# Kernel tuning notes

Hardware: AMD Instinct MI355X
Metric: run time of the kernel (lower is better)

The kernel has to match this reference:

```python
import jax, jax.numpy as jnp
import numpy as np

N, K, D = 8192, 4096, 256


def setup_inputs() -> dict:
    key = jax.random.key(0)
    kx, kc, kw = jax.random.split(key, 3)
    x = jax.random.normal(kx, (N, D), dtype=jnp.float32)
    centers = jax.random.normal(kc, (K, D), dtype=jnp.float32)
    w = jax.random.normal(kw, (K,), dtype=jnp.float32)
    # bandwidth chosen so exp(-sigma * d2) stays in a healthy range for
    # Gaussian data where E[||x-c||^2] ~= 2*D
    sigma = jnp.asarray(1.0 / (2.0 * D), dtype=jnp.float32)
    return {"x": x, "centers": centers, "w": w, "sigma": sigma}


def reference(x, centers, w, sigma):
    # phi[n,k] = exp(-sigma * ||x_n - c_k||^2), computed via the GEMM
    x2 = jnp.sum(x * x, axis=-1, keepdims=True)          # [N,1]
    c2 = jnp.sum(centers * centers, axis=-1)             # [K]
    d2 = x2 + c2 - 2.0 * jnp.einsum('nd,kd->nk', x, centers)  # [N,K]
    d2 = jnp.maximum(d2, 0.0)  # clamp tiny negative round-off
    phi = jnp.exp(-sigma * d2)                           # [N,K]
    # (w * phi).sum(1) == phi @ w
    return jnp.einsum('nk,k->n', phi, w)                 # [N]
```

## Files before the change

### kernel.cpp

```cpp
#include <hip/hip_runtime.h>

#define NROWS 8192
#define NCENT 4096
#define DIM   256

#define AS1 __attribute__((address_space(1)))
#define AS3 __attribute__((address_space(3)))

typedef short bf16x8 __attribute__((ext_vector_type(8)));
typedef float f32x4  __attribute__((ext_vector_type(4)));

__device__ inline unsigned short f2bf(float f) {
    unsigned u = __float_as_uint(f);
    return (unsigned short)((u + 0x7fffu + ((u >> 16) & 1u)) >> 16);
}

__global__ __launch_bounds__(256) void prep_kernel(const float* __restrict__ x,
                                                   const float* __restrict__ c,
                                                   float* __restrict__ norms,
                                                   unsigned short* __restrict__ xbf,
                                                   unsigned short* __restrict__ cbf,
                                                   float* __restrict__ out) {
    const int t = threadIdx.x, lane = t & 63;
    if (blockIdx.x < NROWS / 256) out[blockIdx.x * 256 + t] = 0.0f;
    const int wbase = (blockIdx.x * 4 + (t >> 6)) * 4;
    #pragma unroll
    for (int rr = 0; rr < 4; ++rr) {
        const int gw = wbase + rr;
        const float* src;
        unsigned short* dst;
        if (gw < NROWS) { src = x + (size_t)gw * DIM;           dst = xbf + (size_t)gw * DIM; }
        else            { src = c + (size_t)(gw - NROWS) * DIM; dst = cbf + (size_t)(gw - NROWS) * DIM; }
        float4 v = ((const float4*)src)[lane];
        ushort4 b;
        b.x = f2bf(v.x); b.y = f2bf(v.y); b.z = f2bf(v.z); b.w = f2bf(v.w);
        ((ushort4*)dst)[lane] = b;
        float s = v.x * v.x + v.y * v.y + v.z * v.z + v.w * v.w;
        #pragma unroll
        for (int m = 32; m; m >>= 1) s += __shfl_xor(s, m);
        if (lane == 0) norms[gw] = s;
    }
}

#define BUFH (128 * 32)

__global__ __launch_bounds__(256, 3) void rbf_mfma(const unsigned short* __restrict__ xbf,
                                                   const unsigned short* __restrict__ cbf,
                                                   const float* __restrict__ w,
                                                   const float* __restrict__ sigp,
                                                   const float* __restrict__ norms,
                                                   float* __restrict__ out) {
    __shared__ __align__(16) short As[2 * BUFH];
    __shared__ __align__(16) short Bs[2 * BUFH];

    const int t    = threadIdx.x;
    const int wave = t >> 6, lane = t & 63;
    const int m0   = blockIdx.y * 128;
    const int n0   = blockIdx.x * 128;
    const int wy   = wave >> 1, wx = wave & 1;
    const int lr   = lane & 15;
    const int g    = lane >> 4;

    const int r_in = lane >> 2;
    const int c_l  = (lane & 3) ^ ((r_in >> 1) & 3);
    const unsigned short* ga0 = xbf + (size_t)(m0 + 32 * wave + r_in) * DIM + c_l * 8;
    const unsigned short* ga1 = ga0 + 16 * DIM;
    const unsigned short* gb0 = cbf + (size_t)(n0 + 32 * wave + r_in) * DIM + c_l * 8;
    const unsigned short* gb1 = gb0 + 16 * DIM;
    short* la0 = As + (32 * wave) * 32;
    short* lb0 = Bs + (32 * wave) * 32;

#define STAGE(buf, kk) do {                                                                  \
        const int ko_ = (kk) * 32;                                                           \
        __builtin_amdgcn_global_load_lds((const AS1 void*)(ga0 + ko_),                       \
                                         (AS3 void*)(la0 + (buf) * BUFH), 16, 0, 0);         \
        __builtin_amdgcn_global_load_lds((const AS1 void*)(ga1 + ko_),                       \
                                         (AS3 void*)(la0 + (buf) * BUFH + 16 * 32), 16, 0, 0);\
        __builtin_amdgcn_global_load_lds((const AS1 void*)(gb0 + ko_),                       \
                                         (AS3 void*)(lb0 + (buf) * BUFH), 16, 0, 0);         \
        __builtin_amdgcn_global_load_lds((const AS1 void*)(gb1 + ko_),                       \
                                         (AS3 void*)(lb0 + (buf) * BUFH + 16 * 32), 16, 0, 0);\
    } while (0)

    int aoff[4], boff[4];
    #pragma unroll
    for (int i = 0; i < 4; ++i) {
        int r = 64 * wy + 16 * i + lr;
        aoff[i] = r * 32 + ((g ^ ((r >> 1) & 3)) * 8);
    }
    #pragma unroll
    for (int j = 0; j < 4; ++j) {
        int r = 64 * wx + 16 * j + lr;
        boff[j] = r * 32 + ((g ^ ((r >> 1) & 3)) * 8);
    }

    f32x4 acc[4][4];
    #pragma unroll
    for (int i = 0; i < 4; ++i)
        #pragma unroll
        for (int j = 0; j < 4; ++j) acc[i][j] = f32x4{0, 0, 0, 0};

    STAGE(0, 0);
    __syncthreads();

    #pragma unroll
    for (int kk = 0; kk < DIM / 32; ++kk) {
        const int cur = kk & 1;
        if (kk < DIM / 32 - 1) STAGE(cur ^ 1, kk + 1);

        const short* Ab = As + cur * BUFH;
        const short* Bb = Bs + cur * BUFH;
        bf16x8 a[4], b[4];
        #pragma unroll
        for (int i = 0; i < 4; ++i) a[i] = *(const bf16x8*)(Ab + aoff[i]);
        #pragma unroll
        for (int j = 0; j < 4; ++j) b[j] = *(const bf16x8*)(Bb + boff[j]);
        #pragma unroll
        for (int i = 0; i < 4; ++i)
            #pragma unroll
            for (int j = 0; j < 4; ++j)
                acc[i][j] = __builtin_amdgcn_mfma_f32_16x16x32_bf16(a[i], b[j], acc[i][j], 0, 0, 0);

        __syncthreads();
    }
#undef STAGE

    const float s2 = sigp[0] * 1.4426950408889634f;
    const float* x2 = norms;
    const float* c2 = norms + NROWS;

    float c2v[4], wv[4];
    #pragma unroll
    for (int j = 0; j < 4; ++j) {
        int n = n0 + 64 * wx + 16 * j + lr;
        c2v[j] = c2[n];
        wv[j]  = w[n];
    }
    float4 x2v[4];
    #pragma unroll
    for (int i = 0; i < 4; ++i)
        x2v[i] = *(const float4*)(x2 + m0 + 64 * wy + 16 * i + 4 * g);

    #pragma unroll
    for (int i = 0; i < 4; ++i) {
        const int mbase = m0 + 64 * wy + 16 * i + 4 * g;
        float rs[4] = {0.f, 0.f, 0.f, 0.f};
        #pragma unroll
        for (int j = 0; j < 4; ++j) {
            #pragma unroll
            for (int r = 0; r < 4; ++r) {
                float x2r = (r == 0) ? x2v[i].x : (r == 1) ? x2v[i].y : (r == 2) ? x2v[i].z : x2v[i].w;
                float d2 = x2r + c2v[j] - 2.0f * acc[i][j][r];
                float e  = fminf(-s2 * d2, 0.0f);
                rs[r] += wv[j] * exp2f(e);
            }
        }
        #pragma unroll
        for (int r = 0; r < 4; ++r) {
            rs[r] += __shfl_xor(rs[r], 1);
            rs[r] += __shfl_xor(rs[r], 2);
            rs[r] += __shfl_xor(rs[r], 4);
            rs[r] += __shfl_xor(rs[r], 8);
        }
        if (lr == 0) {
            #pragma unroll
            for (int r = 0; r < 4; ++r) atomicAdd(&out[mbase + r], rs[r]);
        }
    }
}

__global__ __launch_bounds__(256) void norms_kernel(const float* __restrict__ x,
                                                    const float* __restrict__ c,
                                                    float* __restrict__ ws) {
    int t = threadIdx.x, lane = t & 63;
    int gw = blockIdx.x * 4 + (t >> 6);
    const float* src;
    float* dst;
    if (gw < NROWS) { src = x + (size_t)gw * DIM;           dst = ws + gw; }
    else            { src = c + (size_t)(gw - NROWS) * DIM; dst = ws + gw; }
    float4 v = ((const float4*)src)[lane];
    float s = v.x * v.x + v.y * v.y + v.z * v.z + v.w * v.w;
    #pragma unroll
    for (int m = 32; m; m >>= 1) s += __shfl_xor(s, m);
    if (lane == 0) *dst = s;
}

__global__ __launch_bounds__(256) void rbf_kernel(const float* __restrict__ x,
                                                  const float* __restrict__ cent,
                                                  const float* __restrict__ w,
                                                  const float* __restrict__ sigp,
                                                  const float* __restrict__ norms,
                                                  float* __restrict__ out) {
    __shared__ __align__(16) short xs[64 * 32];
    __shared__ __align__(16) short cs[64 * 32];
    const int t = threadIdx.x;
    const int m0 = blockIdx.y * 64, n0 = blockIdx.x * 64;
    const int srow = t >> 2, seg = t & 3;
    const int pchunk = seg ^ ((srow >> 1) & 3);
    const int sidx = srow * 32 + pchunk * 8;
    const float* xg = x    + (size_t)(m0 + srow) * DIM + seg * 8;
    const float* cg = cent + (size_t)(n0 + srow) * DIM + seg * 8;
    const int lane = t & 63, wave = t >> 6;
    const int lr = lane & 15, lg = lane >> 4;
    const int arow = 16 * wave + lr;
    const int aidx = arow * 32 + ((lg ^ ((arow >> 1) & 3)) * 8);
    f32x4 acc[4] = {f32x4{0,0,0,0}, f32x4{0,0,0,0}, f32x4{0,0,0,0}, f32x4{0,0,0,0}};
    for (int k0 = 0; k0 < DIM; k0 += 32) {
        float4 f0 = *(const float4*)(xg + k0);
        float4 f1 = *(const float4*)(xg + k0 + 4);
        float4 g0 = *(const float4*)(cg + k0);
        float4 g1 = *(const float4*)(cg + k0 + 4);
        __syncthreads();
        union { unsigned short s[8]; int4 v; } ux, uc;
        ux.s[0]=f2bf(f0.x); ux.s[1]=f2bf(f0.y); ux.s[2]=f2bf(f0.z); ux.s[3]=f2bf(f0.w);
        ux.s[4]=f2bf(f1.x); ux.s[5]=f2bf(f1.y); ux.s[6]=f2bf(f1.z); ux.s[7]=f2bf(f1.w);
        uc.s[0]=f2bf(g0.x); uc.s[1]=f2bf(g0.y); uc.s[2]=f2bf(g0.z); uc.s[3]=f2bf(g0.w);
        uc.s[4]=f2bf(g1.x); uc.s[5]=f2bf(g1.y); uc.s[6]=f2bf(g1.z); uc.s[7]=f2bf(g1.w);
        *(int4*)(xs + sidx) = ux.v;
        *(int4*)(cs + sidx) = uc.v;
        __syncthreads();
        bf16x8 a = *(const bf16x8*)(xs + aidx);
        #pragma unroll
        for (int bt = 0; bt < 4; ++bt) {
            const int brow = 16 * bt + lr;
            bf16x8 b = *(const bf16x8*)(cs + brow * 32 + ((lg ^ ((brow >> 1) & 3)) * 8));
            acc[bt] = __builtin_amdgcn_mfma_f32_16x16x32_bf16(a, b, acc[bt], 0, 0, 0);
        }
    }
    const float sigma = sigp[0];
    const float* x2 = norms;
    const float* c2 = norms + NROWS;
    const int rbase = m0 + 16 * wave + lg * 4;
    float x2v[4];
    #pragma unroll
    for (int r = 0; r < 4; ++r) x2v[r] = x2[rbase + r];
    float rs[4] = {0.f, 0.f, 0.f, 0.f};
    #pragma unroll
    for (int bt = 0; bt < 4; ++bt) {
        const int col = n0 + 16 * bt + lr;
        const float c2v = c2[col];
        const float wvv = w[col];
        #pragma unroll
        for (int r = 0; r < 4; ++r) {
            float d2 = x2v[r] + c2v - 2.0f * acc[bt][r];
            d2 = fmaxf(d2, 0.0f);
            rs[r] += wvv * __expf(-sigma * d2);
        }
    }
    #pragma unroll
    for (int r = 0; r < 4; ++r) {
        rs[r] += __shfl_xor(rs[r], 1);
        rs[r] += __shfl_xor(rs[r], 2);
        rs[r] += __shfl_xor(rs[r], 4);
        rs[r] += __shfl_xor(rs[r], 8);
    }
    if (lr == 0) {
        #pragma unroll
        for (int r = 0; r < 4; ++r) atomicAdd(&out[rbase + r], rs[r]);
    }
}

extern "C" void kernel_launch(void* const* d_in, const int* in_sizes, int n_in,
                              void* d_out, int out_size, void* d_ws, size_t ws_size,
                              hipStream_t stream) {
    const float* x    = (const float*)d_in[0];
    const float* cent = (const float*)d_in[1];
    const float* w    = (const float*)d_in[2];
    const float* sig  = (const float*)d_in[3];
    float* out = (float*)d_out;

    const size_t norms_elems = NROWS + NCENT;
    const size_t xbf_off  = norms_elems * sizeof(float);
    const size_t cbf_off  = xbf_off + (size_t)NROWS * DIM * sizeof(unsigned short);
    const size_t ws_need  = cbf_off + (size_t)NCENT * DIM * sizeof(unsigned short);

    if (ws_size >= ws_need) {
        float* norms = (float*)d_ws;
        unsigned short* xbf = (unsigned short*)((char*)d_ws + xbf_off);
        unsigned short* cbf = (unsigned short*)((char*)d_ws + cbf_off);
        prep_kernel<<<(NROWS + NCENT) / 16, 256, 0, stream>>>(x, cent, norms, xbf, cbf, out);
        rbf_mfma<<<dim3(NCENT / 128, NROWS / 128), 256, 0, stream>>>(xbf, cbf, w, sig, norms, out);
    } else {
        float* norms = (float*)d_ws;
        hipMemsetAsync(d_out, 0, (size_t)out_size * sizeof(float), stream);
        norms_kernel<<<(NROWS + NCENT) / 4, 256, 0, stream>>>(x, cent, norms);
        rbf_kernel<<<dim3(NCENT / 64, NROWS / 64), 256, 0, stream>>>(x, cent, w, sig, norms, out);
    }
}
```

Before: 108.8 us.

## Load MFMA operands directly from global memory into registers, dropping LDS staging

Removes the shared-memory double buffer and the global_load_lds staging. Each wave now loads its bf16 A/B fragments straight from global memory into registers, with a two-deep register ping-pong across K steps. This eliminates LDS traffic and the per-step barriers, but each wave re-fetches data that other waves in the block used to share. Global loads become 16-byte per-lane row-strided accesses that lean on L1/L2 for reuse.

```diff
diff --git a/kernel.cpp b/kernel.cpp
--- a/kernel.cpp
+++ b/kernel.cpp
@@ -3,9 +3,6 @@
 #define NROWS 8192
 #define NCENT 4096
 #define DIM   256
-
-#define AS1 __attribute__((address_space(1)))
-#define AS3 __attribute__((address_space(3)))
 
 typedef short bf16x8 __attribute__((ext_vector_type(8)));
 typedef float f32x4  __attribute__((ext_vector_type(4)));
@@ -42,17 +39,12 @@
     }
 }
 
-#define BUFH (128 * 32)
-
 __global__ __launch_bounds__(256, 3) void rbf_mfma(const unsigned short* __restrict__ xbf,
                                                    const unsigned short* __restrict__ cbf,
                                                    const float* __restrict__ w,
                                                    const float* __restrict__ sigp,
                                                    const float* __restrict__ norms,
                                                    float* __restrict__ out) {
-    __shared__ __align__(16) short As[2 * BUFH];
-    __shared__ __align__(16) short Bs[2 * BUFH];
-
     const int t    = threadIdx.x;
     const int wave = t >> 6, lane = t & 63;
     const int m0   = blockIdx.y * 128;
@@ -61,38 +53,14 @@
     const int lr   = lane & 15;
     const int g    = lane >> 4;
 
-    const int r_in = lane >> 2;
-    const int c_l  = (lane & 3) ^ ((r_in >> 1) & 3);
-    const unsigned short* ga0 = xbf + (size_t)(m0 + 32 * wave + r_in) * DIM + c_l * 8;
-    const unsigned short* ga1 = ga0 + 16 * DIM;
-    const unsigned short* gb0 = cbf + (size_t)(n0 + 32 * wave + r_in) * DIM + c_l * 8;
-    const unsigned short* gb1 = gb0 + 16 * DIM;
-    short* la0 = As + (32 * wave) * 32;
-    short* lb0 = Bs + (32 * wave) * 32;
-
-#define STAGE(buf, kk) do {                                                                  \
-        const int ko_ = (kk) * 32;                                                           \
-        __builtin_amdgcn_global_load_lds((const AS1 void*)(ga0 + ko_),                       \
-                                         (AS3 void*)(la0 + (buf) * BUFH), 16, 0, 0);         \
-        __builtin_amdgcn_global_load_lds((const AS1 void*)(ga1 + ko_),                       \
-                                         (AS3 void*)(la0 + (buf) * BUFH + 16 * 32), 16, 0, 0);\
-        __builtin_amdgcn_global_load_lds((const AS1 void*)(gb0 + ko_),                       \
-                                         (AS3 void*)(lb0 + (buf) * BUFH), 16, 0, 0);         \
-        __builtin_amdgcn_global_load_lds((const AS1 void*)(gb1 + ko_),                       \
-                                         (AS3 void*)(lb0 + (buf) * BUFH + 16 * 32), 16, 0, 0);\
-    } while (0)
-
-    int aoff[4], boff[4];
-    #pragma unroll
-    for (int i = 0; i < 4; ++i) {
-        int r = 64 * wy + 16 * i + lr;
-        aoff[i] = r * 32 + ((g ^ ((r >> 1) & 3)) * 8);
-    }
-    #pragma unroll
-    for (int j = 0; j < 4; ++j) {
-        int r = 64 * wx + 16 * j + lr;
-        boff[j] = r * 32 + ((g ^ ((r >> 1) & 3)) * 8);
-    }
+    const unsigned short* ga[4];
+    const unsigned short* gb[4];
+    #pragma unroll
+    for (int i = 0; i < 4; ++i)
+        ga[i] = xbf + (size_t)(m0 + 64 * wy + 16 * i + lr) * DIM + g * 8;
+    #pragma unroll
+    for (int j = 0; j < 4; ++j)
+        gb[j] = cbf + (size_t)(n0 + 64 * wx + 16 * j + lr) * DIM + g * 8;
 
     f32x4 acc[4][4];
     #pragma unroll
@@ -100,30 +68,39 @@
         #pragma unroll
         for (int j = 0; j < 4; ++j) acc[i][j] = f32x4{0, 0, 0, 0};
 
-    STAGE(0, 0);
-    __syncthreads();
-
-    #pragma unroll
-    for (int kk = 0; kk < DIM / 32; ++kk) {
-        const int cur = kk & 1;
-        if (kk < DIM / 32 - 1) STAGE(cur ^ 1, kk + 1);
-
-        const short* Ab = As + cur * BUFH;
-        const short* Bb = Bs + cur * BUFH;
-        bf16x8 a[4], b[4];
-        #pragma unroll
-        for (int i = 0; i < 4; ++i) a[i] = *(const bf16x8*)(Ab + aoff[i]);
-        #pragma unroll
-        for (int j = 0; j < 4; ++j) b[j] = *(const bf16x8*)(Bb + boff[j]);
+    bf16x8 a0[4], b0[4], a1[4], b1[4];
+
+    #pragma unroll
+    for (int i = 0; i < 4; ++i) a0[i] = *(const bf16x8*)(ga[i]);
+    #pragma unroll
+    for (int j = 0; j < 4; ++j) b0[j] = *(const bf16x8*)(gb[j]);
+
+    #pragma unroll
+    for (int kk = 0; kk < 8; kk += 2) {
+        if (kk + 1 < 8) {
+            #pragma unroll
+            for (int i = 0; i < 4; ++i) a1[i] = *(const bf16x8*)(ga[i] + (kk + 1) * 32);
+            #pragma unroll
+            for (int j = 0; j < 4; ++j) b1[j] = *(const bf16x8*)(gb[j] + (kk + 1) * 32);
+        }
         #pragma unroll
         for (int i = 0; i < 4; ++i)
             #pragma unroll
             for (int j = 0; j < 4; ++j)
-                acc[i][j] = __builtin_amdgcn_mfma_f32_16x16x32_bf16(a[i], b[j], acc[i][j], 0, 0, 0);
-
-        __syncthreads();
-    }
-#undef STAGE
+                acc[i][j] = __builtin_amdgcn_mfma_f32_16x16x32_bf16(a0[i], b0[j], acc[i][j], 0, 0, 0);
+
+        if (kk + 2 < 8) {
+            #pragma unroll
+            for (int i = 0; i < 4; ++i) a0[i] = *(const bf16x8*)(ga[i] + (kk + 2) * 32);
+            #pragma unroll
+            for (int j = 0; j < 4; ++j) b0[j] = *(const bf16x8*)(gb[j] + (kk + 2) * 32);
+        }
+        #pragma unroll
+        for (int i = 0; i < 4; ++i)
+            #pragma unroll
+            for (int j = 0; j < 4; ++j)
+                acc[i][j] = __builtin_amdgcn_mfma_f32_16x16x32_bf16(a1[i], b1[j], acc[i][j], 0, 0, 0);
+    }
 
     const float s2 = sigp[0] * 1.4426950408889634f;
     const float* x2 = norms;
```

New measurement: 147.6 us. 1.36x slower.
